# Optimization experiments

Hardware: AMD Instinct MI355X
Metric: run time of the kernel (lower is better)

## Reference

```python
import jax, jax.numpy as jnp
import numpy as np


def setup_inputs() -> dict:
    key = jax.random.key(0)
    ks = jax.random.split(key, 8)
    B, S, H = 4, 2048, 1024
    heads = 16
    lim = 1.0 / np.sqrt(H)  # nn.Linear default init range
    x = jax.random.normal(ks[0], (B, S, H), dtype=jnp.float32)
    atten_mask = jnp.zeros((B, 1, S, 1), dtype=jnp.float32)  # 1.0 marks padded positions
    Wq = jax.random.uniform(ks[1], (H, H), jnp.float32, -lim, lim)
    bq = jax.random.uniform(ks[2], (H,), jnp.float32, -lim, lim)
    Wk = jax.random.uniform(ks[3], (H, H), jnp.float32, -lim, lim)
    bk = jax.random.uniform(ks[4], (H,), jnp.float32, -lim, lim)
    Wv = jax.random.uniform(ks[5], (H, H), jnp.float32, -lim, lim)
    bv = jax.random.uniform(ks[6], (H,), jnp.float32, -lim, lim)
    return {"x": x, "Wq": Wq, "bq": bq, "Wk": Wk, "bk": bk, "Wv": Wv, "bv": bv,
            "atten_mask": atten_mask, "attention_head_num": 16}


def reference(x, Wq, bq, Wk, bk, Wv, bv, atten_mask, attention_head_num):
    B, S, H = x.shape
    h = attention_head_num
    d = H // h
    # QKV projections (torch Linear: x @ W.T + b)
    q = (x @ Wq.T + bq).reshape(B, S, h, d).transpose(0, 2, 1, 3)  # [B,h,S,d]
    k = (x @ Wk.T + bk).reshape(B, S, h, d).transpose(0, 2, 1, 3)
    v = (x @ Wv.T + bv).reshape(B, S, h, d).transpose(0, 2, 1, 3)
    # combined padding + look-ahead mask: True -> masked
    causal = jnp.triu(jnp.ones((S, S), dtype=atten_mask.dtype), 1)  # [S,S]
    mask = (atten_mask + causal) >= 1.0  # [B,1 or h,S,S] broadcast
    mask = jnp.broadcast_to(mask, (B, h, S, S))
    scale = 1.0 / jnp.sqrt(jnp.asarray(d, dtype=jnp.float32))
    scores = jnp.einsum('bhqd,bhkd->bhqk', q, k) * scale
    scores = jnp.where(mask, jnp.float32(-1e9), scores)
    att = jax.nn.softmax(scores, axis=-1)
    out = jnp.einsum('bhqk,bhkd->bhqd', att, v)  # [B,h,S,d]
    return out.transpose(0, 2, 1, 3).reshape(B, S, H)
```

## Files before the change

### kernel.cpp

```cpp
#include <hip/hip_runtime.h>
#include <hip/hip_bf16.h>
#include <stdint.h>

typedef short v8s __attribute__((ext_vector_type(8)));
typedef float v4f __attribute__((ext_vector_type(4)));
typedef unsigned long long u64;
typedef unsigned short u16;
typedef unsigned int u32;
typedef u64 v2u __attribute__((ext_vector_type(2)));

__device__ __forceinline__ u16 f2bf(float f) {
    unsigned u = __builtin_bit_cast(unsigned, f);
    u += 0x7FFFu + ((u >> 16) & 1u);
    return (u16)(u >> 16);
}

__device__ __forceinline__ u32 cvt_pk_bf16(float lo, float hi) {
    u32 r;
    asm("v_cvt_pk_bf16_f32 %0, %1, %2" : "=v"(r) : "v"(lo), "v"(hi));
    return r;
}

__device__ __forceinline__ float ex2(float x) {
    float r;
    asm("v_exp_f32 %0, %1" : "=v"(r) : "v"(x));
    return r;
}

__device__ __forceinline__ void gload_lds16(const void* g, const void* lds) {
    __builtin_amdgcn_global_load_lds(
        (const __attribute__((address_space(1))) unsigned int*)(unsigned long long)g,
        (__attribute__((address_space(3))) unsigned int*)(unsigned int)(unsigned long long)lds,
        16, 0, 0);
}

__global__ __launch_bounds__(256) void cvt_bf16(const float* __restrict__ in,
                                                u16* __restrict__ out, int n4) {
    int i = blockIdx.x * 256 + threadIdx.x;
    if (i < n4) {
        float4 v = ((const float4*)in)[i];
        ((ushort4*)out)[i] = make_ushort4(f2bf(v.x), f2bf(v.y), f2bf(v.z), f2bf(v.w));
    }
}

template <int MODE>
__global__ __launch_bounds__(256, 2)
void qkv_gemm(const u16* __restrict__ X, const u16* __restrict__ W,
              const float* __restrict__ bias, u16* __restrict__ Out) {
    __shared__ __align__(16) char smem[34816];
    char* ldsA = smem;
    char* ldsB = smem + 16384;
    u16*  ldsE = (u16*)smem;

    const int t = threadIdx.x;
    const int lane = t & 63, wave = t >> 6;
    const int lhi = lane >> 4, llo = lane & 15;
    const int wm = wave >> 1, wn = wave & 1;
    const int m0 = (blockIdx.x >> 3) * 128;
    const int n0 = (blockIdx.x & 7) * 128;

    v4f acc[4][4] = {};

    for (int k0 = 0; k0 < 1024; k0 += 64) {
        #pragma unroll
        for (int i = 0; i < 4; ++i) {
            int o = (i * 256 + t) * 16;
            int row = o >> 7, c = (o >> 4) & 7;
            const char* wbaseA = ldsA + (i * 256 + wave * 64) * 16;
            const char* wbaseB = ldsB + (i * 256 + wave * 64) * 16;
            gload_lds16(X + (m0 + row) * 1024 + k0 + c * 8, wbaseA);
            gload_lds16(W + (n0 + row) * 1024 + k0 + c * 8, wbaseB);
        }
        __syncthreads();
        #pragma unroll
        for (int s = 0; s < 2; ++s) {
            v8s af[4], bf[4];
            #pragma unroll
            for (int i = 0; i < 4; ++i)
                af[i] = *(const v8s*)(ldsA + (wm * 64 + i * 16 + llo) * 128 + (lhi + 4 * s) * 16);
            #pragma unroll
            for (int j = 0; j < 4; ++j)
                bf[j] = *(const v8s*)(ldsB + (wn * 64 + j * 16 + llo) * 128 + (lhi + 4 * s) * 16);
            #pragma unroll
            for (int i = 0; i < 4; ++i)
                #pragma unroll
                for (int j = 0; j < 4; ++j)
                    acc[i][j] = __builtin_amdgcn_mfma_f32_16x16x32_bf16(af[i], bf[j], acc[i][j], 0, 0, 0);
        }
        __syncthreads();
    }

    float bv_[4];
    #pragma unroll
    for (int j = 0; j < 4; ++j) bv_[j] = bias[n0 + wn * 64 + j * 16 + llo];

    #pragma unroll
    for (int i = 0; i < 4; ++i) {
        #pragma unroll
        for (int j = 0; j < 4; ++j) {
            #pragma unroll
            for (int r = 0; r < 4; ++r) {
                int ml = wm * 64 + i * 16 + lhi * 4 + r;
                int nl = wn * 64 + j * 16 + llo;
                float v = acc[i][j][r] + bv_[j];
                if (MODE == 0) v *= 0.18033688011112042f;
                u16 hh = f2bf(v);
                if (MODE == 2) ldsE[nl * 136 + ml] = hh;
                else           ldsE[ml * 136 + nl] = hh;
            }
        }
    }
    __syncthreads();

    const int row = t >> 1, half = t & 1;
    if (MODE == 2) {
        int n = n0 + row, hh = n >> 6, dd = n & 63;
        int b = m0 >> 11, sbase = (m0 & 2047) + half * 64;
        u16* dst = Out + ((b * 16 + hh) * 64 + dd) * 2048 + sbase;
        #pragma unroll
        for (int j = 0; j < 8; ++j)
            *(v8s*)(dst + j * 8) = *(const v8s*)&ldsE[row * 136 + half * 64 + j * 8];
    } else {
        int m = m0 + row, b = m >> 11, s = m & 2047;
        int hh = (n0 + half * 64) >> 6;
        u16* dst = Out + ((b * 16 + hh) * 2048 + s) * 64;
        #pragma unroll
        for (int j = 0; j < 8; ++j)
            *(v8s*)(dst + j * 8) = *(const v8s*)&ldsE[row * 136 + half * 64 + j * 8];
    }
}

__global__ __launch_bounds__(256, 4)
void flash_attn(const u16* __restrict__ Qg, const u16* __restrict__ Kg,
                const u16* __restrict__ VTg, const float* __restrict__ am,
                float* __restrict__ out) {
    __shared__ __align__(16) char smem[25088];
    char* ldsK = smem;
    char* ldsV = smem + 8192;
    char* ldsP = smem + 16384 + (threadIdx.x >> 6) * 2176;

    const int t = threadIdx.x;
    const int lane = t & 63, wave = t >> 6;
    const int lhi = lane >> 4, llo = lane & 15;
    const int bh = blockIdx.x;
    const int qi = 31 - blockIdx.y;
    const int b = bh >> 4, h = bh & 15;
    const int q0 = qi * 64;
    const int qw = q0 + wave * 16;
    const int q = qw + llo;

    v8s qf[2];
    #pragma unroll
    for (int s = 0; s < 2; ++s)
        qf[s] = *(const v8s*)(Qg + (bh * 2048 + q) * 64 + lhi * 8 + 32 * s);

    const float rowpen = am[b * 2048 + q];

    float mrow = -1e30f, lrow = 0.f;
    v4f o_acc[4] = {};

    for (int kj = 0; kj <= qi; ++kj) {
        const int kv0 = kj * 64;
        #pragma unroll
        for (int i = 0; i < 2; ++i) {
            int o = (i * 256 + t) * 16;
            int row = o >> 7, sc = (o >> 4) & 7;
            int c = sc ^ (row & 7);
            const char* wbK = ldsK + (i * 256 + wave * 64) * 16;
            const char* wbV = ldsV + (i * 256 + wave * 64) * 16;
            gload_lds16(Kg + (bh * 2048 + kv0 + row) * 64 + c * 8, wbK);
            gload_lds16(VTg + (bh * 64 + row) * 2048 + kv0 + c * 8, wbV);
        }
        __syncthreads();

        const int nt4 = (kj == qi) ? (wave + 1) : 4;
        v4f sacc[4] = {};
        #pragma unroll
        for (int tt = 0; tt < 4; ++tt) {
            if (tt < nt4) {
                #pragma unroll
                for (int s = 0; s < 2; ++s) {
                    int row = tt * 16 + llo;
                    int c = lhi + 4 * s;
                    v8s kb = *(const v8s*)(ldsK + row * 128 + ((c ^ (row & 7)) << 4));
                    sacc[tt] = __builtin_amdgcn_mfma_f32_16x16x32_bf16(kb, qf[s], sacc[tt], 0, 0, 0);
                }
            }
        }

        if (kj == qi) {
            #pragma unroll
            for (int tt = 0; tt < 4; ++tt)
                #pragma unroll
                for (int r = 0; r < 4; ++r) {
                    int kvg = kv0 + tt * 16 + lhi * 4 + r;
                    if (kvg > q) sacc[tt][r] = -1e30f;
                }
        }
        if (rowpen >= 1.0f) {
            #pragma unroll
            for (int tt = 0; tt < 4; ++tt)
                #pragma unroll
                for (int r = 0; r < 4; ++r) sacc[tt][r] = -1e30f;
        }

        float mx = fmaxf(fmaxf(sacc[0][0], sacc[0][1]), fmaxf(sacc[0][2], sacc[0][3]));
        #pragma unroll
        for (int tt = 1; tt < 4; ++tt) {
            float m2 = fmaxf(fmaxf(sacc[tt][0], sacc[tt][1]), fmaxf(sacc[tt][2], sacc[tt][3]));
            mx = fmaxf(mx, m2);
        }
        mx = fmaxf(mx, __shfl_xor(mx, 16));
        mx = fmaxf(mx, __shfl_xor(mx, 32));
        const float mn = fmaxf(mrow, mx);
        const float sc_o = ex2(mrow - mn);
        mrow = mn;

        float rs = 0.f;
        #pragma unroll
        for (int tt = 0; tt < 4; ++tt) {
            float p0 = ex2(sacc[tt][0] - mn);
            float p1 = ex2(sacc[tt][1] - mn);
            float p2 = ex2(sacc[tt][2] - mn);
            float p3 = ex2(sacc[tt][3] - mn);
            rs += (p0 + p1) + (p2 + p3);
            u32 w0 = cvt_pk_bf16(p0, p1);
            u32 w1 = cvt_pk_bf16(p2, p3);
            *(u64*)(ldsP + llo * 136 + tt * 32 + lhi * 8) = (u64)w0 | ((u64)w1 << 32);
        }
        rs += __shfl_xor(rs, 16);
        rs += __shfl_xor(rs, 32);
        lrow = lrow * sc_o + rs;

        #pragma unroll
        for (int dt = 0; dt < 4; ++dt)
            #pragma unroll
            for (int r = 0; r < 4; ++r) o_acc[dt][r] *= sc_o;

        #pragma unroll
        for (int s = 0; s < 2; ++s) {
            u64 plo = *(const u64*)(ldsP + llo * 136 + lhi * 16 + s * 64);
            u64 phi = *(const u64*)(ldsP + llo * 136 + lhi * 16 + s * 64 + 8);
            v2u tmp; tmp.x = plo; tmp.y = phi;
            v8s pb = __builtin_bit_cast(v8s, tmp);
            #pragma unroll
            for (int dt = 0; dt < 4; ++dt) {
                int vrow = dt * 16 + llo;
                v8s vb = *(const v8s*)(ldsV + vrow * 128 + (((lhi + 4 * s) ^ (vrow & 7)) << 4));
                o_acc[dt] = __builtin_amdgcn_mfma_f32_16x16x32_bf16(vb, pb, o_acc[dt], 0, 0, 0);
            }
        }
        __syncthreads();
    }

    const float inv = 1.0f / lrow;
    float* dst = out + (size_t)(b * 2048 + q) * 1024 + h * 64 + lhi * 4;
    #pragma unroll
    for (int dt = 0; dt < 4; ++dt) {
        float4 o;
        o.x = o_acc[dt][0] * inv;
        o.y = o_acc[dt][1] * inv;
        o.z = o_acc[dt][2] * inv;
        o.w = o_acc[dt][3] * inv;
        *(float4*)(dst + dt * 16) = o;
    }
}

extern "C" void kernel_launch(void* const* d_in, const int* in_sizes, int n_in,
                              void* d_out, int out_size, void* d_ws, size_t ws_size,
                              hipStream_t stream) {
    const float* x  = (const float*)d_in[0];
    const float* Wq = (const float*)d_in[1];
    const float* bq = (const float*)d_in[2];
    const float* Wk = (const float*)d_in[3];
    const float* bk = (const float*)d_in[4];
    const float* Wv = (const float*)d_in[5];
    const float* bv = (const float*)d_in[6];
    const float* amask = (const float*)d_in[7];
    float* out = (float*)d_out;

    char* ws = (char*)d_ws;
    u16* xb  = (u16*)(ws);
    u16* Wqb = (u16*)(ws + 16777216);
    u16* Wkb = (u16*)(ws + 16777216 + 2097152);
    u16* Wvb = (u16*)(ws + 16777216 + 2 * 2097152);
    u16* Qg  = (u16*)(ws + 23068672);
    u16* Kg  = (u16*)(ws + 39845888);
    u16* VTg = (u16*)(ws + 56623104);

    cvt_bf16<<<8192, 256, 0, stream>>>(x, xb, 2097152);
    cvt_bf16<<<1024, 256, 0, stream>>>(Wq, Wqb, 262144);
    cvt_bf16<<<1024, 256, 0, stream>>>(Wk, Wkb, 262144);
    cvt_bf16<<<1024, 256, 0, stream>>>(Wv, Wvb, 262144);

    qkv_gemm<0><<<512, 256, 0, stream>>>(xb, Wqb, bq, Qg);
    qkv_gemm<1><<<512, 256, 0, stream>>>(xb, Wkb, bk, Kg);
    qkv_gemm<2><<<512, 256, 0, stream>>>(xb, Wvb, bv, VTg);

    flash_attn<<<dim3(64, 32), 256, 0, stream>>>(Qg, Kg, VTg, amask, out);
}
```

Baseline: 178.9 us.

## Merge conversion and QKV launches, double-buffer KV tiles, lazy softmax rescale

```diff
diff --git a/kernel.cpp b/kernel.cpp
--- a/kernel.cpp
+++ b/kernel.cpp
@@ -34,30 +34,45 @@
         16, 0, 0);
 }
 
-__global__ __launch_bounds__(256) void cvt_bf16(const float* __restrict__ in,
-                                                u16* __restrict__ out, int n4) {
+__global__ __launch_bounds__(256) void cvt_all(const float* __restrict__ x,
+                                               const float* __restrict__ wq,
+                                               const float* __restrict__ wk,
+                                               const float* __restrict__ wv,
+                                               u16* __restrict__ xb, u16* __restrict__ wqb,
+                                               u16* __restrict__ wkb, u16* __restrict__ wvb) {
     int i = blockIdx.x * 256 + threadIdx.x;
-    if (i < n4) {
-        float4 v = ((const float4*)in)[i];
-        ((ushort4*)out)[i] = make_ushort4(f2bf(v.x), f2bf(v.y), f2bf(v.z), f2bf(v.w));
-    }
-}
-
-template <int MODE>
+    const float* in;
+    u16* out;
+    if (i < 2097152)      { in = x;  out = xb; }
+    else if (i < 2359296) { in = wq; out = wqb; i -= 2097152; }
+    else if (i < 2621440) { in = wk; out = wkb; i -= 2359296; }
+    else                  { in = wv; out = wvb; i -= 2621440; }
+    float4 v = ((const float4*)in)[i];
+    ((ushort4*)out)[i] = make_ushort4(f2bf(v.x), f2bf(v.y), f2bf(v.z), f2bf(v.w));
+}
+
 __global__ __launch_bounds__(256, 2)
-void qkv_gemm(const u16* __restrict__ X, const u16* __restrict__ W,
-              const float* __restrict__ bias, u16* __restrict__ Out) {
+void qkv_gemm_all(const u16* __restrict__ X,
+                  const u16* __restrict__ Wq, const u16* __restrict__ Wk, const u16* __restrict__ Wv,
+                  const float* __restrict__ bq, const float* __restrict__ bk, const float* __restrict__ bv,
+                  u16* __restrict__ Qg, u16* __restrict__ Kg, u16* __restrict__ VTg) {
     __shared__ __align__(16) char smem[34816];
     char* ldsA = smem;
     char* ldsB = smem + 16384;
     u16*  ldsE = (u16*)smem;
 
+    const int mode = blockIdx.x >> 9;
+    const int bx = blockIdx.x & 511;
+    const u16* W = (mode == 0) ? Wq : (mode == 1) ? Wk : Wv;
+    const float* bias = (mode == 0) ? bq : (mode == 1) ? bk : bv;
+    u16* Out = (mode == 0) ? Qg : (mode == 1) ? Kg : VTg;
+
     const int t = threadIdx.x;
     const int lane = t & 63, wave = t >> 6;
     const int lhi = lane >> 4, llo = lane & 15;
     const int wm = wave >> 1, wn = wave & 1;
-    const int m0 = (blockIdx.x >> 3) * 128;
-    const int n0 = (blockIdx.x & 7) * 128;
+    const int m0 = (bx >> 3) * 128;
+    const int n0 = (bx & 7) * 128;
 
     v4f acc[4][4] = {};
 
@@ -72,6 +87,7 @@
             gload_lds16(W + (n0 + row) * 1024 + k0 + c * 8, wbaseB);
         }
         __syncthreads();
+        __builtin_amdgcn_s_setprio(1);
         #pragma unroll
         for (int s = 0; s < 2; ++s) {
             v8s af[4], bf[4];
@@ -87,12 +103,14 @@
                 for (int j = 0; j < 4; ++j)
                     acc[i][j] = __builtin_amdgcn_mfma_f32_16x16x32_bf16(af[i], bf[j], acc[i][j], 0, 0, 0);
         }
+        __builtin_amdgcn_s_setprio(0);
         __syncthreads();
     }
 
     float bv_[4];
     #pragma unroll
     for (int j = 0; j < 4; ++j) bv_[j] = bias[n0 + wn * 64 + j * 16 + llo];
+    const float scl = (mode == 0) ? 0.18033688011112042f : 1.0f;
 
     #pragma unroll
     for (int i = 0; i < 4; ++i) {
@@ -102,10 +120,9 @@
             for (int r = 0; r < 4; ++r) {
                 int ml = wm * 64 + i * 16 + lhi * 4 + r;
                 int nl = wn * 64 + j * 16 + llo;
-                float v = acc[i][j][r] + bv_[j];
-                if (MODE == 0) v *= 0.18033688011112042f;
+                float v = (acc[i][j][r] + bv_[j]) * scl;
                 u16 hh = f2bf(v);
-                if (MODE == 2) ldsE[nl * 136 + ml] = hh;
+                if (mode == 2) ldsE[nl * 136 + ml] = hh;
                 else           ldsE[ml * 136 + nl] = hh;
             }
         }
@@ -113,7 +130,7 @@
     __syncthreads();
 
     const int row = t >> 1, half = t & 1;
-    if (MODE == 2) {
+    if (mode == 2) {
         int n = n0 + row, hh = n >> 6, dd = n & 63;
         int b = m0 >> 11, sbase = (m0 & 2047) + half * 64;
         u16* dst = Out + ((b * 16 + hh) * 64 + dd) * 2048 + sbase;
@@ -130,14 +147,14 @@
     }
 }
 
-__global__ __launch_bounds__(256, 4)
+__global__ __launch_bounds__(256, 3)
 void flash_attn(const u16* __restrict__ Qg, const u16* __restrict__ Kg,
                 const u16* __restrict__ VTg, const float* __restrict__ am,
                 float* __restrict__ out) {
-    __shared__ __align__(16) char smem[25088];
+    __shared__ __align__(16) char smem[41472];
     char* ldsK = smem;
-    char* ldsV = smem + 8192;
-    char* ldsP = smem + 16384 + (threadIdx.x >> 6) * 2176;
+    char* ldsV = smem + 16384;
+    char* ldsP = smem + 32768 + (threadIdx.x >> 6) * 2176;
 
     const int t = threadIdx.x;
     const int lane = t & 63, wave = t >> 6;
@@ -145,8 +162,7 @@
     const int bh = blockIdx.x;
     const int qi = 31 - blockIdx.y;
     const int b = bh >> 4, h = bh & 15;
-    const int q0 = qi * 64;
-    const int qw = q0 + wave * 16;
+    const int qw = qi * 64 + wave * 16;
     const int q = qw + llo;
 
     v8s qf[2];
@@ -156,25 +172,34 @@
 
     const float rowpen = am[b * 2048 + q];
 
+    const int srow = (t * 16) >> 7, ssc = ((t * 16) >> 4) & 7;
+    const int sc1 = ssc ^ (srow & 7), sc2 = ssc ^ ((srow + 32) & 7);
+    #define STAGE(buf, kj2) do {                                                   \
+        const int kv0_ = (kj2) * 64;                                               \
+        const char* wbK = ldsK + (buf) * 8192 + (wave * 64) * 16;                  \
+        const char* wbV = ldsV + (buf) * 8192 + (wave * 64) * 16;                  \
+        gload_lds16(Kg + (bh * 2048 + kv0_ + srow) * 64 + sc1 * 8, wbK);           \
+        gload_lds16(VTg + (bh * 64 + srow) * 2048 + kv0_ + sc1 * 8, wbV);          \
+        gload_lds16(Kg + (bh * 2048 + kv0_ + srow + 32) * 64 + sc2 * 8, wbK + 4096); \
+        gload_lds16(VTg + (bh * 64 + srow + 32) * 2048 + kv0_ + sc2 * 8, wbV + 4096); \
+    } while (0)
+
     float mrow = -1e30f, lrow = 0.f;
     v4f o_acc[4] = {};
 
+    STAGE(0, 0);
+    __syncthreads();
+
     for (int kj = 0; kj <= qi; ++kj) {
+        const int cur = kj & 1;
+        if (kj < qi) STAGE(cur ^ 1, kj + 1);
+        const char* K = ldsK + cur * 8192;
+        const char* V = ldsV + cur * 8192;
         const int kv0 = kj * 64;
-        #pragma unroll
-        for (int i = 0; i < 2; ++i) {
-            int o = (i * 256 + t) * 16;
-            int row = o >> 7, sc = (o >> 4) & 7;
-            int c = sc ^ (row & 7);
-            const char* wbK = ldsK + (i * 256 + wave * 64) * 16;
-            const char* wbV = ldsV + (i * 256 + wave * 64) * 16;
-            gload_lds16(Kg + (bh * 2048 + kv0 + row) * 64 + c * 8, wbK);
-            gload_lds16(VTg + (bh * 64 + row) * 2048 + kv0 + c * 8, wbV);
-        }
-        __syncthreads();
 
         const int nt4 = (kj == qi) ? (wave + 1) : 4;
         v4f sacc[4] = {};
+        __builtin_amdgcn_s_setprio(1);
         #pragma unroll
         for (int tt = 0; tt < 4; ++tt) {
             if (tt < nt4) {
@@ -182,11 +207,12 @@
                 for (int s = 0; s < 2; ++s) {
                     int row = tt * 16 + llo;
                     int c = lhi + 4 * s;
-                    v8s kb = *(const v8s*)(ldsK + row * 128 + ((c ^ (row & 7)) << 4));
+                    v8s kb = *(const v8s*)(K + row * 128 + ((c ^ (row & 7)) << 4));
                     sacc[tt] = __builtin_amdgcn_mfma_f32_16x16x32_bf16(kb, qf[s], sacc[tt], 0, 0, 0);
                 }
             }
         }
+        __builtin_amdgcn_s_setprio(0);
 
         if (kj == qi) {
             #pragma unroll
@@ -206,23 +232,29 @@
 
         float mx = fmaxf(fmaxf(sacc[0][0], sacc[0][1]), fmaxf(sacc[0][2], sacc[0][3]));
         #pragma unroll
-        for (int tt = 1; tt < 4; ++tt) {
-            float m2 = fmaxf(fmaxf(sacc[tt][0], sacc[tt][1]), fmaxf(sacc[tt][2], sacc[tt][3]));
-            mx = fmaxf(mx, m2);
-        }
+        for (int tt = 1; tt < 4; ++tt)
+            mx = fmaxf(mx, fmaxf(fmaxf(sacc[tt][0], sacc[tt][1]), fmaxf(sacc[tt][2], sacc[tt][3])));
         mx = fmaxf(mx, __shfl_xor(mx, 16));
         mx = fmaxf(mx, __shfl_xor(mx, 32));
-        const float mn = fmaxf(mrow, mx);
-        const float sc_o = ex2(mrow - mn);
-        mrow = mn;
+
+        if (__any(mx > mrow + 8.0f)) {
+            const float mn = fmaxf(mrow, mx);
+            const float sc_o = ex2(mrow - mn);
+            mrow = mn;
+            lrow *= sc_o;
+            #pragma unroll
+            for (int dt = 0; dt < 4; ++dt)
+                #pragma unroll
+                for (int r = 0; r < 4; ++r) o_acc[dt][r] *= sc_o;
+        }
 
         float rs = 0.f;
         #pragma unroll
         for (int tt = 0; tt < 4; ++tt) {
-            float p0 = ex2(sacc[tt][0] - mn);
-            float p1 = ex2(sacc[tt][1] - mn);
-            float p2 = ex2(sacc[tt][2] - mn);
-            float p3 = ex2(sacc[tt][3] - mn);
+            float p0 = ex2(sacc[tt][0] - mrow);
+            float p1 = ex2(sacc[tt][1] - mrow);
+            float p2 = ex2(sacc[tt][2] - mrow);
+            float p3 = ex2(sacc[tt][3] - mrow);
             rs += (p0 + p1) + (p2 + p3);
             u32 w0 = cvt_pk_bf16(p0, p1);
             u32 w1 = cvt_pk_bf16(p2, p3);
@@ -230,13 +262,9 @@
         }
         rs += __shfl_xor(rs, 16);
         rs += __shfl_xor(rs, 32);
-        lrow = lrow * sc_o + rs;
-
-        #pragma unroll
-        for (int dt = 0; dt < 4; ++dt)
-            #pragma unroll
-            for (int r = 0; r < 4; ++r) o_acc[dt][r] *= sc_o;
-
+        lrow += rs;
+
+        __builtin_amdgcn_s_setprio(1);
         #pragma unroll
         for (int s = 0; s < 2; ++s) {
             u64 plo = *(const u64*)(ldsP + llo * 136 + lhi * 16 + s * 64);
@@ -246,10 +274,11 @@
             #pragma unroll
             for (int dt = 0; dt < 4; ++dt) {
                 int vrow = dt * 16 + llo;
-                v8s vb = *(const v8s*)(ldsV + vrow * 128 + (((lhi + 4 * s) ^ (vrow & 7)) << 4));
+                v8s vb = *(const v8s*)(V + vrow * 128 + (((lhi + 4 * s) ^ (vrow & 7)) << 4));
                 o_acc[dt] = __builtin_amdgcn_mfma_f32_16x16x32_bf16(vb, pb, o_acc[dt], 0, 0, 0);
             }
         }
+        __builtin_amdgcn_s_setprio(0);
         __syncthreads();
     }
 
@@ -288,14 +317,7 @@
     u16* Kg  = (u16*)(ws + 39845888);
     u16* VTg = (u16*)(ws + 56623104);
 
-    cvt_bf16<<<8192, 256, 0, stream>>>(x, xb, 2097152);
-    cvt_bf16<<<1024, 256, 0, stream>>>(Wq, Wqb, 262144);
-    cvt_bf16<<<1024, 256, 0, stream>>>(Wk, Wkb, 262144);
-    cvt_bf16<<<1024, 256, 0, stream>>>(Wv, Wvb, 262144);
-
-    qkv_gemm<0><<<512, 256, 0, stream>>>(xb, Wqb, bq, Qg);
-    qkv_gemm<1><<<512, 256, 0, stream>>>(xb, Wkb, bk, Kg);
-    qkv_gemm<2><<<512, 256, 0, stream>>>(xb, Wvb, bv, VTg);
-
+    cvt_all<<<11264, 256, 0, stream>>>(x, Wq, Wk, Wv, xb, Wqb, Wkb, Wvb);
+    qkv_gemm_all<<<1536, 256, 0, stream>>>(xb, Wqb, Wkb, Wvb, bq, bk, bv, Qg, Kg, VTg);
     flash_attn<<<dim3(64, 32), 256, 0, stream>>>(Qg, Kg, VTg, amask, out);
 }
```

Result: faster. 164.5 us (-8.1%).
